# Optimization experiments

Measured on AMD Instinct MI355X. Metric: run time of the kernel, lower is better.

The kernel has to match this reference:

```python
import jax, jax.numpy as jnp
import numpy as np

S = 7
B = 2
C = 20
COORD = 5.0
NOOBJ = 0.5
N_IMG = 16384
SS = S * S
F = B * 5 + C  # 30


def setup_inputs() -> dict:
    key = jax.random.key(0)
    k1, k2, k3, k4 = jax.random.split(key, 4)
    preds = jax.random.uniform(k1, (N_IMG, SS, F), dtype=jnp.float32)
    # targets built per the YOLOv1 encoding described in the docstring
    t_probs = jax.random.uniform(k2, (N_IMG, SS, C), dtype=jnp.float32)
    obj = jax.random.bernoulli(k3, 0.3, (N_IMG, SS))
    t_conf = jnp.where(obj[..., None], 1.0, -1.0) * jnp.ones((N_IMG, SS, B), jnp.float32)
    t_box = jax.random.uniform(k4, (N_IMG, SS, B * 4), dtype=jnp.float32,
                               minval=0.05, maxval=1.0)
    t_box = jnp.where(obj[..., None], t_box, 0.0)
    targets = jnp.concatenate([t_probs, t_conf, t_box], axis=-1)
    return {"preds": preds, "targets": targets}


def _iou(pb, tb):
    # pb, tb: (N, SS, B, 4) as (cx, cy, w, h) -> (N, SS, B)
    xA = jnp.maximum(pb[..., 0] - pb[..., 2] / 2, tb[..., 0] - tb[..., 2] / 2)
    yA = jnp.maximum(pb[..., 1] - pb[..., 3] / 2, tb[..., 1] - tb[..., 3] / 2)
    xB = jnp.minimum(pb[..., 0] + pb[..., 2] / 2, tb[..., 0] + tb[..., 2] / 2)
    yB = jnp.minimum(pb[..., 1] + pb[..., 3] / 2, tb[..., 1] + tb[..., 3] / 2)
    inter = jnp.maximum(0.0, xB - xA) * jnp.maximum(0.0, yB - yA)
    areaA = pb[..., 2] * pb[..., 3]
    areaB = tb[..., 2] * tb[..., 3]
    return inter / (areaA + areaB - inter)


def reference(preds, targets):
    N = preds.shape[0]
    p_probs = preds[..., :C]
    p_conf = preds[..., C:C + B]
    p_box = preds[..., C + B:].reshape(N, SS, B, 4)
    t_probs = targets[..., :C]
    t_conf = targets[..., C:C + B]
    t_box = targets[..., C + B:].reshape(N, SS, B, 4)

    obj = t_conf[..., 0] > 0  # (N, SS)

    # no-obj weighted confidence SSE over ALL cells (original adds it unconditionally)
    loss = NOOBJ * jnp.sum((p_conf - t_conf) ** 2)

    # class-prob SSE only at object cells
    loss = loss + jnp.sum(jnp.where(obj, jnp.sum((p_probs - t_probs) ** 2, axis=-1), 0.0))

    # IoU-based responsible-box selection (original computes IoU via numpy -> no grad)
    scores = jax.lax.stop_gradient(_iou(p_box, t_box))  # (N, SS, B)
    best = jnp.argmax(scores, axis=-1)  # (N, SS)

    # extra confidence term for the responsible box
    pc = jnp.take_along_axis(p_conf, best[..., None], axis=-1)[..., 0]
    tc = jnp.take_along_axis(t_conf, best[..., None], axis=-1)[..., 0]
    loss = loss + (1.0 - NOOBJ) * jnp.sum(jnp.where(obj, (pc - tc) ** 2, 0.0))

    # coordinate loss for the responsible box
    pb = jnp.take_along_axis(p_box, best[..., None, None], axis=-2)[..., 0, :]  # (N, SS, 4)
    tb = jnp.take_along_axis(t_box, best[..., None, None], axis=-2)[..., 0, :]
    # guard sqrt at no-obj cells (target w/h are 0 there; masked out of the loss)
    tb_wh = jnp.where(obj[..., None], tb[..., 2:4], 1.0)
    bl = ((pb[..., 0] - tb[..., 0]) ** 2
          + (pb[..., 1] - tb[..., 1]) ** 2
          + (jnp.sqrt(pb[..., 2]) - jnp.sqrt(tb_wh[..., 0])) ** 2
          + (jnp.sqrt(pb[..., 3]) - jnp.sqrt(tb_wh[..., 1])) ** 2)
    loss = loss + COORD * jnp.sum(jnp.where(obj, bl, 0.0))

    return loss / N
```

## Files before the change

kernel.cpp:

```cpp
#include <hip/hip_runtime.h>

#define S_      7
#define SS_     49
#define B_      2
#define C_      20
#define F_      30
#define N_IMG_  16384
#define NCELL_  (N_IMG_ * SS_)
#define COORD_  5.0f
#define NOOBJ_  0.5f

#define TPB           256
#define CELLS_PER_BLK TPB
#define NBLK          (NCELL_ / CELLS_PER_BLK)
#define FLT_PER_BLK   (CELLS_PER_BLK * F_)
#define VEC4_PER_BLK  (FLT_PER_BLK / 4)

typedef const __attribute__((address_space(1))) void g_void;
typedef __attribute__((address_space(3))) void lds_void;

__device__ __forceinline__ float iou_f(const float* pb, const float* tb) {
    float xA = fmaxf(pb[0] - pb[2] * 0.5f, tb[0] - tb[2] * 0.5f);
    float yA = fmaxf(pb[1] - pb[3] * 0.5f, tb[1] - tb[3] * 0.5f);
    float xB = fminf(pb[0] + pb[2] * 0.5f, tb[0] + tb[2] * 0.5f);
    float yB = fminf(pb[1] + pb[3] * 0.5f, tb[1] + tb[3] * 0.5f);
    float inter = fmaxf(0.f, xB - xA) * fmaxf(0.f, yB - yA);
    float areaA = pb[2] * pb[3];
    float areaB = tb[2] * tb[3];
    return inter / (areaA + areaB - inter);
}

__global__ __launch_bounds__(TPB) void mploss_kernel(
        const float* __restrict__ preds,
        const float* __restrict__ targets,
        float* __restrict__ out) {
    __shared__ alignas(16) float s_p[FLT_PER_BLK];
    __shared__ alignas(16) float s_t[FLT_PER_BLK];
    __shared__ float s_red[TPB / 64];

    const int tid  = threadIdx.x;
    const int lane = tid & 63;
    const int wave = tid >> 6;

    const float4* p4 = (const float4*)preds   + (long)blockIdx.x * VEC4_PER_BLK;
    const float4* t4 = (const float4*)targets + (long)blockIdx.x * VEC4_PER_BLK;

    for (int c = wave; c < 30; c += 4) {
        __builtin_amdgcn_global_load_lds(
            (g_void*)(p4 + c * 64 + lane),
            (lds_void*)(s_p + c * 256), 16, 0, 0);
        __builtin_amdgcn_global_load_lds(
            (g_void*)(t4 + c * 64 + lane),
            (lds_void*)(s_t + c * 256), 16, 0, 0);
    }
    __syncthreads();

    const float* p = s_p + tid * F_;
    const float* q = s_t + tid * F_;

    float l = 0.f;

    {
        float d0 = p[20] - q[20];
        float d1 = p[21] - q[21];
        l += NOOBJ_ * (d0 * d0 + d1 * d1);
    }

    const bool obj = q[20] > 0.f;
    if (obj) {
        float sprob = 0.f;
        #pragma unroll
        for (int f = 0; f < C_; ++f) {
            float d = p[f] - q[f];
            sprob += d * d;
        }
        l += sprob;

        float i0 = iou_f(p + 22, q + 22);
        float i1 = iou_f(p + 26, q + 26);
        int best = (i1 > i0) ? 1 : 0;

        float dc = p[20 + best] - q[20 + best];
        l += (1.0f - NOOBJ_) * dc * dc;

        const float* pb = p + 22 + 4 * best;
        const float* tb = q + 22 + 4 * best;
        float bx = pb[0] - tb[0];
        float by = pb[1] - tb[1];
        float bw = sqrtf(pb[2]) - sqrtf(tb[2]);
        float bh = sqrtf(pb[3]) - sqrtf(tb[3]);
        l += COORD_ * (bx * bx + by * by + bw * bw + bh * bh);
    }

    #pragma unroll
    for (int off = 32; off > 0; off >>= 1)
        l += __shfl_down(l, off, 64);

    if (lane == 0) s_red[wave] = l;
    __syncthreads();
    if (tid == 0) {
        float tot = s_red[0] + s_red[1] + s_red[2] + s_red[3];
        atomicAdd(out, tot * (1.0f / (float)N_IMG_));
    }
}

extern "C" void kernel_launch(void* const* d_in, const int* in_sizes, int n_in,
                              void* d_out, int out_size, void* d_ws, size_t ws_size,
                              hipStream_t stream) {
    const float* preds   = (const float*)d_in[0];
    const float* targets = (const float*)d_in[1];
    float* out = (float*)d_out;

    hipMemsetAsync(out, 0, sizeof(float) * (size_t)out_size, stream);

    mploss_kernel<<<NBLK, TPB, 0, stream>>>(preds, targets, out);
}
```

Before: 205.4 us.

## Load cell pairs straight into registers with float4 loads instead of LDS staging

Drops the global-to-LDS async staging and has each thread load two consecutive cells (60 floats, 15 float4) directly from global memory into registers, then compute both cell losses. This removes the LDS buffers and the block-wide barrier after staging, and halves the block count. Each thread's float4 loads hit addresses 240 bytes apart, so coalescing across a wave is poorer, and the kernel now holds 120 floats per thread in registers, which raises register pressure. The launch bound adds a minimum of 3 blocks per CU as an occupancy hint.

```diff
diff --git a/kernel.cpp b/kernel.cpp
--- a/kernel.cpp
+++ b/kernel.cpp
@@ -10,64 +10,28 @@
 #define COORD_  5.0f
 #define NOOBJ_  0.5f
 
-#define TPB           256
-#define CELLS_PER_BLK TPB
-#define NBLK          (NCELL_ / CELLS_PER_BLK)
-#define FLT_PER_BLK   (CELLS_PER_BLK * F_)
-#define VEC4_PER_BLK  (FLT_PER_BLK / 4)
+#define TPB            256
+#define CELLS_PER_THR  2
+#define NBLK           (NCELL_ / (TPB * CELLS_PER_THR))
 
-typedef const __attribute__((address_space(1))) void g_void;
-typedef __attribute__((address_space(3))) void lds_void;
-
-__device__ __forceinline__ float iou_f(const float* pb, const float* tb) {
-    float xA = fmaxf(pb[0] - pb[2] * 0.5f, tb[0] - tb[2] * 0.5f);
-    float yA = fmaxf(pb[1] - pb[3] * 0.5f, tb[1] - tb[3] * 0.5f);
-    float xB = fminf(pb[0] + pb[2] * 0.5f, tb[0] + tb[2] * 0.5f);
-    float yB = fminf(pb[1] + pb[3] * 0.5f, tb[1] + tb[3] * 0.5f);
+__device__ __forceinline__ float iou8(float px, float py, float pw, float ph,
+                                      float tx, float ty, float tw, float th) {
+    float xA = fmaxf(px - pw * 0.5f, tx - tw * 0.5f);
+    float yA = fmaxf(py - ph * 0.5f, ty - th * 0.5f);
+    float xB = fminf(px + pw * 0.5f, tx + tw * 0.5f);
+    float yB = fminf(py + ph * 0.5f, ty + th * 0.5f);
     float inter = fmaxf(0.f, xB - xA) * fmaxf(0.f, yB - yA);
-    float areaA = pb[2] * pb[3];
-    float areaB = tb[2] * tb[3];
+    float areaA = pw * ph;
+    float areaB = tw * th;
     return inter / (areaA + areaB - inter);
 }
 
-__global__ __launch_bounds__(TPB) void mploss_kernel(
-        const float* __restrict__ preds,
-        const float* __restrict__ targets,
-        float* __restrict__ out) {
-    __shared__ alignas(16) float s_p[FLT_PER_BLK];
-    __shared__ alignas(16) float s_t[FLT_PER_BLK];
-    __shared__ float s_red[TPB / 64];
+__device__ __forceinline__ float cell_loss(const float* p, const float* q) {
+    float d0 = p[20] - q[20];
+    float d1 = p[21] - q[21];
+    float l = NOOBJ_ * (d0 * d0 + d1 * d1);
 
-    const int tid  = threadIdx.x;
-    const int lane = tid & 63;
-    const int wave = tid >> 6;
-
-    const float4* p4 = (const float4*)preds   + (long)blockIdx.x * VEC4_PER_BLK;
-    const float4* t4 = (const float4*)targets + (long)blockIdx.x * VEC4_PER_BLK;
-
-    for (int c = wave; c < 30; c += 4) {
-        __builtin_amdgcn_global_load_lds(
-            (g_void*)(p4 + c * 64 + lane),
-            (lds_void*)(s_p + c * 256), 16, 0, 0);
-        __builtin_amdgcn_global_load_lds(
-            (g_void*)(t4 + c * 64 + lane),
-            (lds_void*)(s_t + c * 256), 16, 0, 0);
-    }
-    __syncthreads();
-
-    const float* p = s_p + tid * F_;
-    const float* q = s_t + tid * F_;
-
-    float l = 0.f;
-
-    {
-        float d0 = p[20] - q[20];
-        float d1 = p[21] - q[21];
-        l += NOOBJ_ * (d0 * d0 + d1 * d1);
-    }
-
-    const bool obj = q[20] > 0.f;
-    if (obj) {
+    if (q[20] > 0.f) {
         float sprob = 0.f;
         #pragma unroll
         for (int f = 0; f < C_; ++f) {
@@ -76,21 +40,54 @@
         }
         l += sprob;
 
-        float i0 = iou_f(p + 22, q + 22);
-        float i1 = iou_f(p + 26, q + 26);
-        int best = (i1 > i0) ? 1 : 0;
+        float i0 = iou8(p[22], p[23], p[24], p[25], q[22], q[23], q[24], q[25]);
+        float i1 = iou8(p[26], p[27], p[28], p[29], q[26], q[27], q[28], q[29]);
+        bool b1 = i1 > i0;
 
-        float dc = p[20 + best] - q[20 + best];
+        float pc = b1 ? p[21] : p[20];
+        float tc = b1 ? q[21] : q[20];
+        float dc = pc - tc;
         l += (1.0f - NOOBJ_) * dc * dc;
 
-        const float* pb = p + 22 + 4 * best;
-        const float* tb = q + 22 + 4 * best;
-        float bx = pb[0] - tb[0];
-        float by = pb[1] - tb[1];
-        float bw = sqrtf(pb[2]) - sqrtf(tb[2]);
-        float bh = sqrtf(pb[3]) - sqrtf(tb[3]);
+        float pb0 = b1 ? p[26] : p[22];
+        float pb1 = b1 ? p[27] : p[23];
+        float pb2 = b1 ? p[28] : p[24];
+        float pb3 = b1 ? p[29] : p[25];
+        float tb0 = b1 ? q[26] : q[22];
+        float tb1 = b1 ? q[27] : q[23];
+        float tb2 = b1 ? q[28] : q[24];
+        float tb3 = b1 ? q[29] : q[25];
+        float bx = pb0 - tb0;
+        float by = pb1 - tb1;
+        float bw = sqrtf(pb2) - sqrtf(tb2);
+        float bh = sqrtf(pb3) - sqrtf(tb3);
         l += COORD_ * (bx * bx + by * by + bw * bw + bh * bh);
     }
+    return l;
+}
+
+__global__ __launch_bounds__(TPB, 3) void mploss_kernel(
+        const float* __restrict__ preds,
+        const float* __restrict__ targets,
+        float* __restrict__ out) {
+    __shared__ float s_red[TPB / 64];
+
+    const int tid  = threadIdx.x;
+    const int lane = tid & 63;
+    const int wave = tid >> 6;
+
+    const long pair = (long)blockIdx.x * TPB + tid;
+    const float4* p4 = (const float4*)preds   + pair * 15;
+    const float4* t4 = (const float4*)targets + pair * 15;
+
+    union { float4 v[15]; float f[60]; } P, T;
+    #pragma unroll
+    for (int i = 0; i < 15; ++i) P.v[i] = p4[i];
+    #pragma unroll
+    for (int i = 0; i < 15; ++i) T.v[i] = t4[i];
+
+    float l = cell_loss(P.f,      T.f)
+            + cell_loss(P.f + 30, T.f + 30);
 
     #pragma unroll
     for (int off = 32; off > 0; off >>= 1)
```

New measurement: 209.9 us. 1.02x slower.
